# Kernel optimization log

Hardware: AMD Instinct MI355X
Metric: run time of the kernel (lower is better)

The kernel has to match this reference:

```python
import jax, jax.numpy as jnp
import numpy as np

N = 50000          # total atoms in batch
E = 1_600_000      # total edges (flattened neighbor list)
ELEM = 64          # elem_fea_len
NBR = 32           # nbr_fea_len
EPS = 1e-5         # BatchNorm eps


def _batchnorm(x, gamma, beta):
    # training-mode BatchNorm1d: per-feature batch stats (biased variance)
    mean = x.mean(axis=0)
    var = ((x - mean) ** 2).mean(axis=0)
    return gamma * (x - mean) * jax.lax.rsqrt(var + EPS) + beta


def setup_inputs() -> dict:
    key = jax.random.key(0)
    ks = jax.random.split(key, 6)
    atom_in_fea = jax.random.normal(ks[0], (N, ELEM), jnp.float32)
    nbr_fea = jax.random.normal(ks[1], (E, NBR), jnp.float32)
    self_fea_idx = jnp.sort(jax.random.randint(ks[2], (E,), 0, N))
    nbr_fea_idx = jax.random.randint(ks[3], (E,), 0, N)
    fan_in = 2 * ELEM + NBR
    W = jax.random.normal(ks[4], (fan_in, 2 * ELEM), jnp.float32) * (1.0 / np.sqrt(fan_in))
    b = jnp.zeros((2 * ELEM,), jnp.float32)
    gamma1 = jnp.ones((2 * ELEM,), jnp.float32)
    beta1 = jnp.zeros((2 * ELEM,), jnp.float32)
    gamma2 = jnp.ones((ELEM,), jnp.float32)
    beta2 = jnp.zeros((ELEM,), jnp.float32)
    return {
        "atom_in_fea": atom_in_fea,
        "nbr_fea": nbr_fea,
        "self_fea_idx": self_fea_idx,
        "nbr_fea_idx": nbr_fea_idx,
        "W": W,
        "b": b,
        "gamma1": gamma1,
        "beta1": beta1,
        "gamma2": gamma2,
        "beta2": beta2,
    }


def reference(atom_in_fea, nbr_fea, self_fea_idx, nbr_fea_idx,
              W, b, gamma1, beta1, gamma2, beta2):
    # gather + concat: (E, 2*ELEM + NBR)
    total_fea = jnp.concatenate(
        [atom_in_fea[self_fea_idx], atom_in_fea[nbr_fea_idx], nbr_fea], axis=1)
    total_fea = total_fea @ W + b                    # fc_full: (E, 2*ELEM)
    total_fea = _batchnorm(total_fea, gamma1, beta1)  # bn1
    filter_fea, core_fea = jnp.split(total_fea, 2, axis=1)
    nbr_msg = jax.nn.sigmoid(filter_fea) * jax.nn.softplus(core_fea)  # (E, ELEM)
    nbr_sumed = jax.ops.segment_sum(nbr_msg, self_fea_idx, num_segments=N)
    nbr_sumed = _batchnorm(nbr_sumed, gamma2, beta2)  # bn2
    return jax.nn.softplus(atom_in_fea + nbr_sumed)   # residual + softplus2
```

## Files before the change

### kernel.cpp

```cpp
#include <hip/hip_runtime.h>

#define E_TOT 1600000
#define N_AT  50000

typedef unsigned short u16;
typedef __attribute__((ext_vector_type(8))) __bf16 bf16x8;
typedef __attribute__((ext_vector_type(4))) __bf16 bf16x4;
typedef __attribute__((ext_vector_type(4))) float f32x4;

#define SUM1_OFF 0
#define SUM2_OFF 1024
#define WF_OFF   2048
#define NS_OFF   43008
#define AB_OFF   12843008
#define NBRB_OFF 19243008

__device__ __forceinline__ u16 f2bf(float f) {
    unsigned int u = __float_as_uint(f);
    return (u16)((u + 0x7FFFu + ((u >> 16) & 1u)) >> 16);
}
__device__ __forceinline__ float softplus_f(float x) {
    return fmaxf(x, 0.0f) + __logf(1.0f + __expf(-fabsf(x)));
}
__device__ __forceinline__ bf16x8 cvt8v(f32x4 a, f32x4 b) {
    bf16x8 r;
    r[0] = (__bf16)a[0]; r[1] = (__bf16)a[1]; r[2] = (__bf16)a[2]; r[3] = (__bf16)a[3];
    r[4] = (__bf16)b[0]; r[5] = (__bf16)b[1]; r[6] = (__bf16)b[2]; r[7] = (__bf16)b[3];
    return r;
}

__global__ __launch_bounds__(256) void k_setup(const float* __restrict__ atom,
                                               const float* __restrict__ W,
                                               char* __restrict__ ws) {
    u16* wf   = (u16*)(ws + WF_OFF);
    float* ns = (float*)(ws + NS_OFF);
    u16* ab   = (u16*)(ws + AB_OFF);
    const int tid = blockIdx.x * 256 + threadIdx.x;
    const int gsz = gridDim.x * 256;

    for (int i = tid; i < 512; i += gsz) ((float*)ws)[i] = 0.0f;

    f32x4 z = {0.f, 0.f, 0.f, 0.f};
    for (int i = tid; i < N_AT * 64 / 4; i += gsz) ((f32x4*)ns)[i] = z;

    for (int i = tid; i < N_AT * 64 / 4; i += gsz) {
        f32x4 v = ((const f32x4*)atom)[i];
        bf16x4 h;
        h[0] = (__bf16)v[0]; h[1] = (__bf16)v[1];
        h[2] = (__bf16)v[2]; h[3] = (__bf16)v[3];
        *(bf16x4*)(ab + i * 4) = h;
    }

    for (int t = tid; t < 20480; t += gsz) {
        int j = t & 7, l2 = (t >> 3) & 63, ct = (t >> 9) & 7, kt = t >> 12;
        int k = kt * 32 + (l2 >> 4) * 8 + j;
        int c = ct * 16 + (l2 & 15);
        wf[t] = f2bf(W[k * 128 + c]);
    }
}

__global__ __launch_bounds__(512, 6) void k1_stats(const u16* __restrict__ ab,
                                                   const float* __restrict__ nbr,
                                                   u16* __restrict__ nbrb,
                                                   const int* __restrict__ sidx,
                                                   const int* __restrict__ nidx,
                                                   const u16* __restrict__ wf,
                                                   float* __restrict__ sums1) {
    __shared__ u16 bsm[20480];
    __shared__ float bs[256];
    const int tx = threadIdx.x, lane = tx & 63, w = tx >> 6;
    const int mrow = lane & 15, quad = lane >> 4;

    const int r0 = blockIdx.x * 128 + w * 16 + mrow;
    const int s0 = sidx[r0];
    const int n0 = nidx[r0];
    const u16* pa0 = ab + (size_t)s0 * 64 + quad * 8;
    const u16* pb0 = ab + (size_t)n0 * 64 + quad * 8;
    const float* p0 = nbr + (size_t)r0 * 32 + quad * 8;

    bf16x8 a0 = *(const bf16x8*)(pa0);
    bf16x8 a1 = *(const bf16x8*)(pa0 + 32);
    bf16x8 a2 = *(const bf16x8*)(pb0);
    bf16x8 a3 = *(const bf16x8*)(pb0 + 32);
    bf16x8 a4 = cvt8v(*(const f32x4*)p0, *(const f32x4*)(p0 + 4));
    *(bf16x8*)(nbrb + (size_t)r0 * 32 + quad * 8) = a4;

    if (tx < 256) bs[tx] = 0.0f;
#pragma unroll
    for (int i = 0; i < 5; i++) {
        int idx = (i * 512 + tx) * 8;
        *(bf16x8*)&bsm[idx] = *(const bf16x8*)&wf[idx];
    }
    __syncthreads();

    f32x4 acc[8];
#pragma unroll
    for (int ct = 0; ct < 8; ct++) { f32x4 z = {0.f, 0.f, 0.f, 0.f}; acc[ct] = z; }

#pragma unroll
    for (int kt = 0; kt < 5; kt++) {
        bf16x8 a = (kt == 0) ? a0 : (kt == 1) ? a1 : (kt == 2) ? a2 : (kt == 3) ? a3 : a4;
#pragma unroll
        for (int ct = 0; ct < 8; ct++) {
            bf16x8 b = *(const bf16x8*)&bsm[((kt * 8 + ct) * 64 + lane) * 8];
            acc[ct] = __builtin_amdgcn_mfma_f32_16x16x32_bf16(a, b, acc[ct], 0, 0, 0);
        }
    }

#pragma unroll
    for (int ct = 0; ct < 8; ct++) {
        float s = 0.f, q = 0.f;
#pragma unroll
        for (int rg = 0; rg < 4; rg++) {
            float v = acc[ct][rg];
            s += v; q += v * v;
        }
        s += __shfl_xor(s, 16, 64); s += __shfl_xor(s, 32, 64);
        q += __shfl_xor(q, 16, 64); q += __shfl_xor(q, 32, 64);
        if (quad == 0) {
            atomicAdd(&bs[ct * 16 + mrow], s);
            atomicAdd(&bs[128 + ct * 16 + mrow], q);
        }
    }
    __syncthreads();
    if (tx < 256) atomicAdd(&sums1[tx], bs[tx]);
}

__global__ __launch_bounds__(512, 6) void k3_msg(const u16* __restrict__ ab,
                                                 const u16* __restrict__ nbrb,
                                                 const int* __restrict__ sidx,
                                                 const int* __restrict__ nidx,
                                                 const u16* __restrict__ wf,
                                                 const float* __restrict__ sums1,
                                                 const float* __restrict__ g1,
                                                 const float* __restrict__ b1,
                                                 float* __restrict__ ns) {
    __shared__ __align__(16) char smraw[40960];
    u16* bsm = (u16*)smraw;
    float (*msgb)[16 * 66] = (float(*)[16 * 66])smraw;
    const int tx = threadIdx.x, lane = tx & 63, w = tx >> 6;
    const int mrow = lane & 15, quad = lane >> 4;

    const int rb = blockIdx.x * 128 + w * 16;
    const int r0 = rb + mrow;
    const int s0 = sidx[r0];
    const int n0 = nidx[r0];
    const u16* pa0 = ab + (size_t)s0 * 64 + quad * 8;
    const u16* pb0 = ab + (size_t)n0 * 64 + quad * 8;

    bf16x8 a0 = *(const bf16x8*)(pa0);
    bf16x8 a1 = *(const bf16x8*)(pa0 + 32);
    bf16x8 a2 = *(const bf16x8*)(pb0);
    bf16x8 a3 = *(const bf16x8*)(pb0 + 32);
    bf16x8 a4 = *(const bf16x8*)(nbrb + (size_t)r0 * 32 + quad * 8);

#pragma unroll
    for (int i = 0; i < 5; i++) {
        int idx = (i * 512 + tx) * 8;
        *(bf16x8*)&bsm[idx] = *(const bf16x8*)&wf[idx];
    }
    __syncthreads();

    f32x4 acc[8];
#pragma unroll
    for (int ct = 0; ct < 8; ct++) { f32x4 z = {0.f, 0.f, 0.f, 0.f}; acc[ct] = z; }

#pragma unroll
    for (int kt = 0; kt < 5; kt++) {
        bf16x8 a = (kt == 0) ? a0 : (kt == 1) ? a1 : (kt == 2) ? a2 : (kt == 3) ? a3 : a4;
#pragma unroll
        for (int ct = 0; ct < 8; ct++) {
            bf16x8 b = *(const bf16x8*)&bsm[((kt * 8 + ct) * 64 + lane) * 8];
            acc[ct] = __builtin_amdgcn_mfma_f32_16x16x32_bf16(a, b, acc[ct], 0, 0, 0);
        }
    }

    const float invE = 1.0f / (float)E_TOT;
    float af[4], kf[4], ac[4], kc[4];
#pragma unroll
    for (int ct = 0; ct < 4; ct++) {
        int cf = ct * 16 + mrow, cc = cf + 64;
        float mf = sums1[cf] * invE;
        float vf = sums1[128 + cf] * invE - mf * mf;
        af[ct] = g1[cf] * rsqrtf(vf + 1e-5f);
        kf[ct] = b1[cf] - af[ct] * mf;
        float mc = sums1[cc] * invE;
        float vc = sums1[128 + cc] * invE - mc * mc;
        ac[ct] = g1[cc] * rsqrtf(vc + 1e-5f);
        kc[ct] = b1[cc] - ac[ct] * mc;
    }

    __syncthreads();

    float* mw = msgb[w];
#pragma unroll
    for (int ct = 0; ct < 4; ct++) {
#pragma unroll
        for (int rg = 0; rg < 4; rg++) {
            float xf = af[ct] * acc[ct][rg] + kf[ct];
            float xc = ac[ct] * acc[ct + 4][rg] + kc[ct];
            float sg = 1.0f / (1.0f + __expf(-xf));
            mw[(quad * 4 + rg) * 66 + ct * 16 + mrow] = sg * softplus_f(xc);
        }
    }

    float accum = 0.f;
    int cur = sidx[rb];
#pragma unroll
    for (int i = 0; i < 16; i++) {
        int idx = sidx[rb + i];
        if (idx != cur) {
            atomicAdd(&ns[(size_t)cur * 64 + lane], accum);
            accum = 0.f;
            cur = idx;
        }
        accum += mw[i * 66 + lane];
    }
    atomicAdd(&ns[(size_t)cur * 64 + lane], accum);
}

__global__ __launch_bounds__(256) void k4_bn2stats(const float* __restrict__ ns,
                                                   float* __restrict__ sums2) {
    const int tx = threadIdx.x;
    const int col = tx & 63, rg = tx >> 6;
    float s = 0.f, q = 0.f;
    for (int r = blockIdx.x * 4 + rg; r < N_AT; r += 256 * 4) {
        float v = ns[r * 64 + col];
        s += v; q += v * v;
    }
    atomicAdd(&sums2[col], s);
    atomicAdd(&sums2[64 + col], q);
}

__global__ __launch_bounds__(256) void k5_final(const float* __restrict__ atom,
                                                const float* __restrict__ ns,
                                                const float* __restrict__ sums2,
                                                const float* __restrict__ g2,
                                                const float* __restrict__ b2,
                                                float* __restrict__ out) {
    const int i = blockIdx.x * 256 + threadIdx.x;
    const int col = i & 63;
    const float invN = 1.0f / (float)N_AT;
    float mean = sums2[col] * invN;
    float var = sums2[64 + col] * invN - mean * mean;
    float a2 = g2[col] * rsqrtf(var + 1e-5f);
    float c2 = b2[col] - a2 * mean;
    out[i] = softplus_f(atom[i] + a2 * ns[i] + c2);
}

extern "C" void kernel_launch(void* const* d_in, const int* in_sizes, int n_in,
                              void* d_out, int out_size, void* d_ws, size_t ws_size,
                              hipStream_t stream) {
    const float* atom = (const float*)d_in[0];
    const float* nbr  = (const float*)d_in[1];
    const int* sidx   = (const int*)d_in[2];
    const int* nidx   = (const int*)d_in[3];
    const float* W    = (const float*)d_in[4];
    const float* g1   = (const float*)d_in[6];
    const float* b1   = (const float*)d_in[7];
    const float* g2   = (const float*)d_in[8];
    const float* b2   = (const float*)d_in[9];
    float* out = (float*)d_out;

    char* ws = (char*)d_ws;
    float* sums1 = (float*)(ws + SUM1_OFF);
    float* sums2 = (float*)(ws + SUM2_OFF);
    u16*   wf    = (u16*)(ws + WF_OFF);
    float* nsum  = (float*)(ws + NS_OFF);
    u16*   ab    = (u16*)(ws + AB_OFF);
    u16*   nbrb  = (u16*)(ws + NBRB_OFF);

    k_setup<<<1024, 256, 0, stream>>>(atom, W, ws);
    k1_stats<<<E_TOT / 128, 512, 0, stream>>>(ab, nbr, nbrb, sidx, nidx, wf, sums1);
    k3_msg<<<E_TOT / 128, 512, 0, stream>>>(ab, nbrb, sidx, nidx, wf, sums1, g1, b1, nsum);
    k4_bn2stats<<<256, 256, 0, stream>>>(nsum, sums2);
    k5_final<<<(N_AT * 64) / 256, 256, 0, stream>>>(atom, nsum, sums2, g2, b2, out);
}
```

Measured before the change: 832.4 us.

## Use direct-to-LDS weight loads and replace global stat atomics with partial reduction

```diff
diff --git a/kernel.cpp b/kernel.cpp
--- a/kernel.cpp
+++ b/kernel.cpp
@@ -2,6 +2,7 @@
 
 #define E_TOT 1600000
 #define N_AT  50000
+#define NB1   (E_TOT / 128)
 
 typedef unsigned short u16;
 typedef __attribute__((ext_vector_type(8))) __bf16 bf16x8;
@@ -14,6 +15,7 @@
 #define NS_OFF   43008
 #define AB_OFF   12843008
 #define NBRB_OFF 19243008
+#define PART_OFF 121643008
 
 __device__ __forceinline__ u16 f2bf(float f) {
     unsigned int u = __float_as_uint(f);
@@ -27,6 +29,11 @@
     r[0] = (__bf16)a[0]; r[1] = (__bf16)a[1]; r[2] = (__bf16)a[2]; r[3] = (__bf16)a[3];
     r[4] = (__bf16)b[0]; r[5] = (__bf16)b[1]; r[6] = (__bf16)b[2]; r[7] = (__bf16)b[3];
     return r;
+}
+__device__ __forceinline__ void ldsdma16(void* lds, const void* g) {
+    __builtin_amdgcn_global_load_lds(
+        (const __attribute__((address_space(1))) unsigned int*)g,
+        (__attribute__((address_space(3))) unsigned int*)lds, 16, 0, 0);
 }
 
 __global__ __launch_bounds__(256) void k_setup(const float* __restrict__ atom,
@@ -65,11 +72,17 @@
                                                    const int* __restrict__ sidx,
                                                    const int* __restrict__ nidx,
                                                    const u16* __restrict__ wf,
-                                                   float* __restrict__ sums1) {
-    __shared__ u16 bsm[20480];
+                                                   float* __restrict__ part) {
+    __shared__ __align__(16) u16 bsm[20480];
     __shared__ float bs[256];
     const int tx = threadIdx.x, lane = tx & 63, w = tx >> 6;
     const int mrow = lane & 15, quad = lane >> 4;
+
+#pragma unroll
+    for (int i = 0; i < 5; i++) {
+        int off = (i * 512 + tx) * 16;
+        ldsdma16((char*)bsm + off, (const char*)wf + off);
+    }
 
     const int r0 = blockIdx.x * 128 + w * 16 + mrow;
     const int s0 = sidx[r0];
@@ -86,11 +99,6 @@
     *(bf16x8*)(nbrb + (size_t)r0 * 32 + quad * 8) = a4;
 
     if (tx < 256) bs[tx] = 0.0f;
-#pragma unroll
-    for (int i = 0; i < 5; i++) {
-        int idx = (i * 512 + tx) * 8;
-        *(bf16x8*)&bsm[idx] = *(const bf16x8*)&wf[idx];
-    }
     __syncthreads();
 
     f32x4 acc[8];
@@ -123,7 +131,15 @@
         }
     }
     __syncthreads();
-    if (tx < 256) atomicAdd(&sums1[tx], bs[tx]);
+    if (tx < 256) part[(size_t)blockIdx.x * 256 + tx] = bs[tx];
+}
+
+__global__ __launch_bounds__(256) void k2_red(const float* __restrict__ part,
+                                              float* __restrict__ sums1) {
+    const int tx = threadIdx.x;
+    float s = 0.f;
+    for (int r = blockIdx.x; r < NB1; r += 256) s += part[(size_t)r * 256 + tx];
+    atomicAdd(&sums1[tx], s);
 }
 
 __global__ __launch_bounds__(512, 6) void k3_msg(const u16* __restrict__ ab,
@@ -141,6 +157,12 @@
     const int tx = threadIdx.x, lane = tx & 63, w = tx >> 6;
     const int mrow = lane & 15, quad = lane >> 4;
 
+#pragma unroll
+    for (int i = 0; i < 5; i++) {
+        int off = (i * 512 + tx) * 16;
+        ldsdma16(smraw + off, (const char*)wf + off);
+    }
+
     const int rb = blockIdx.x * 128 + w * 16;
     const int r0 = rb + mrow;
     const int s0 = sidx[r0];
@@ -154,11 +176,6 @@
     bf16x8 a3 = *(const bf16x8*)(pb0 + 32);
     bf16x8 a4 = *(const bf16x8*)(nbrb + (size_t)r0 * 32 + quad * 8);
 
-#pragma unroll
-    for (int i = 0; i < 5; i++) {
-        int idx = (i * 512 + tx) * 8;
-        *(bf16x8*)&bsm[idx] = *(const bf16x8*)&wf[idx];
-    }
     __syncthreads();
 
     f32x4 acc[8];
@@ -269,10 +286,12 @@
     float* nsum  = (float*)(ws + NS_OFF);
     u16*   ab    = (u16*)(ws + AB_OFF);
     u16*   nbrb  = (u16*)(ws + NBRB_OFF);
+    float* part  = (float*)(ws + PART_OFF);
 
     k_setup<<<1024, 256, 0, stream>>>(atom, W, ws);
-    k1_stats<<<E_TOT / 128, 512, 0, stream>>>(ab, nbr, nbrb, sidx, nidx, wf, sums1);
-    k3_msg<<<E_TOT / 128, 512, 0, stream>>>(ab, nbrb, sidx, nidx, wf, sums1, g1, b1, nsum);
+    k1_stats<<<NB1, 512, 0, stream>>>(ab, nbr, nbrb, sidx, nidx, wf, part);
+    k2_red<<<256, 256, 0, stream>>>(part, sums1);
+    k3_msg<<<NB1, 512, 0, stream>>>(ab, nbrb, sidx, nidx, wf, sums1, g1, b1, nsum);
     k4_bn2stats<<<256, 256, 0, stream>>>(nsum, sums2);
     k5_final<<<(N_AT * 64) / 256, 256, 0, stream>>>(atom, nsum, sums2, g2, b2, out);
 }
```

Measured after the change: 709.2 us. -14.8%, faster.
